# Performance work log

Measured on AMD Instinct MI355X. Metric: run time of the kernel, lower is better.

The kernel has to match this reference:

```python
import jax, jax.numpy as jnp
import numpy as np

NUM_CLASSES = 32
MAX_DET = 100        # max_detections
CONF = 0.25          # conf_threshold
IOU_THR = 0.45       # iou_threshold
BATCH = 64
ANCHORS = 8400


def setup_inputs() -> dict:
    key = jax.random.key(0)
    # raw YOLO head output [B, 4+num_classes, anchors]; uniform [0,1) so boxes
    # (normalized cx,cy,w,h) and class scores are in valid range.
    yolo_output = jax.random.uniform(key, (BATCH, 4 + NUM_CLASSES, ANCHORS), dtype=jnp.float32)
    return {"yolo_output": yolo_output}


def _iou_one_vs_all(box, boxes):
    # box: [4] (ymin,xmin,ymax,xmax); boxes: [A,4]
    y1 = jnp.maximum(box[0], boxes[:, 0])
    x1 = jnp.maximum(box[1], boxes[:, 1])
    y2 = jnp.minimum(box[2], boxes[:, 2])
    x2 = jnp.minimum(box[3], boxes[:, 3])
    inter = jnp.maximum(y2 - y1, 0.0) * jnp.maximum(x2 - x1, 0.0)
    area_a = (box[2] - box[0]) * (box[3] - box[1])
    area_b = (boxes[:, 2] - boxes[:, 0]) * (boxes[:, 3] - boxes[:, 1])
    union = area_a + area_b - inter
    return jnp.where(union > 0.0, inter / union, 0.0)


def _nms_one_image(boxes, classes, scores):
    # Greedy hard NMS, equivalent to tf.image.non_max_suppression followed by
    # gather + zero-pad to MAX_DET. `scores` already has sub-threshold anchors
    # masked to -1 (emulating boolean_mask by threshold).
    def step(sc, _):
        idx = jnp.argmax(sc)
        s = sc[idx]
        b = boxes[idx]
        c = classes[idx]
        ok = s > 0.0  # any remaining valid candidate?
        iou = _iou_one_vs_all(b, boxes)
        new_sc = jnp.where(iou > IOU_THR, -1.0, sc).at[idx].set(-1.0)
        sc = jnp.where(ok, new_sc, sc)
        out = (jnp.where(ok, b, 0.0), jnp.where(ok, c, 0.0), jnp.where(ok, s, 0.0), ok)
        return sc, out

    _, (sel_boxes, sel_classes, sel_scores, valid) = jax.lax.scan(
        step, scores, None, length=MAX_DET)
    num_det = jnp.sum(valid.astype(jnp.float32))
    return sel_boxes, sel_classes, sel_scores, num_det


def _forward(yolo_output):
    # [B, 36, A] -> [B, A, 36]
    t = jnp.transpose(yolo_output, (0, 2, 1))
    boxes_raw = t[..., :4]                      # cx, cy, w, h (normalized)
    class_scores = t[..., 4:]                   # [B, A, num_classes]
    best_scores = jnp.max(class_scores, axis=-1)
    best_classes = jax.lax.stop_gradient(
        jnp.argmax(class_scores, axis=-1).astype(jnp.float32))
    xc, yc, w, h = (boxes_raw[..., 0], boxes_raw[..., 1],
                    boxes_raw[..., 2], boxes_raw[..., 3])
    clip = lambda v: jnp.clip(v, 0.0, 1.0)
    # TF order: [ymin, xmin, ymax, xmax]
    corner = jnp.stack([clip(yc - h * 0.5), clip(xc - w * 0.5),
                        clip(yc + h * 0.5), clip(xc + w * 0.5)], axis=-1)
    # confidence threshold: mask out instead of boolean_mask (jit-friendly)
    masked_scores = jnp.where(best_scores >= CONF, best_scores, -1.0)
    det_boxes, det_classes, det_scores, num_det = jax.vmap(_nms_one_image)(
        corner, best_classes, masked_scores)
    return det_boxes, det_classes, det_scores, num_det


def reference(yolo_output):
    # Returns (detection_boxes [B,100,4], detection_classes [B,100],
    #          detection_scores [B,100], num_detections [B])
    return _forward(yolo_output)
```

## Files before the change

kernel.cpp:

```cpp
#include <hip/hip_runtime.h>

#define BATCH   64
#define CHANS   36
#define ANCH    8400
#define NCLS    32
#define MAXDET  100
#define CONF    0.25f
#define KTOP    512
#define NBUCK   2048
#define BUCK0   (0x3E800000u >> 13)

typedef unsigned long long u64;
typedef unsigned int       u32;

__device__ __forceinline__ bool iou_gt(float ay1, float ax1, float ay2, float ax2, float aar,
                                       float by1, float bx1, float by2, float bx2, float bar,
                                       double M) {
#pragma clang fp contract(off)
    float iy1 = fmaxf(ay1, by1), ix1 = fmaxf(ax1, bx1);
    float iy2 = fminf(ay2, by2), ix2 = fminf(ax2, bx2);
    float inter = fmaxf(iy2 - iy1, 0.f) * fmaxf(ix2 - ix1, 0.f);
    float uni = (aar + bar) - inter;
    return (double)inter > M * (double)uni;
}

__global__ __launch_bounds__(256) void yolo_prep(const float* __restrict__ in,
                                                 float4* __restrict__ wbox,
                                                 u64* __restrict__ wk64,
                                                 u32* __restrict__ hist) {
#pragma clang fp contract(off)
    const int G = ANCH / 4;
    int g = blockIdx.x * 256 + threadIdx.x;
    int b = blockIdx.y;
    bool act = (g < G);

    __shared__ u32 lh[NBUCK];
    for (int i = threadIdx.x; i < NBUCK; i += 256) lh[i] = 0u;
    __syncthreads();

    if (act) {
        const float4* p = (const float4*)(in + (size_t)b * (CHANS * ANCH));
        float4 xc = p[0 * G + g], yc = p[1 * G + g], ww = p[2 * G + g], hh = p[3 * G + g];
        float4 best = p[4 * G + g];
        uint4 bc = make_uint4(0, 0, 0, 0);
#pragma unroll
        for (int k = 1; k < NCLS; ++k) {
            float4 v = p[(4 + k) * G + g];
            if (v.x > best.x) { best.x = v.x; bc.x = k; }
            if (v.y > best.y) { best.y = v.y; bc.y = k; }
            if (v.z > best.z) { best.z = v.z; bc.z = k; }
            if (v.w > best.w) { best.w = v.w; bc.w = k; }
        }
        int a0 = b * ANCH + 4 * g;
        u64* wk = wk64 + (size_t)b * ANCH + 4 * g;
#define PREP_C(C, I)                                                          \
        {                                                                     \
            float Y1 = fminf(fmaxf(yc.C - hh.C * 0.5f, 0.f), 1.f);            \
            float X1 = fminf(fmaxf(xc.C - ww.C * 0.5f, 0.f), 1.f);            \
            float Y2 = fminf(fmaxf(yc.C + hh.C * 0.5f, 0.f), 1.f);            \
            float X2 = fminf(fmaxf(xc.C + ww.C * 0.5f, 0.f), 1.f);            \
            wbox[a0 + I] = make_float4(Y1, X1, Y2, X2);                       \
            u64 kv = 0ull;                                                    \
            if (best.C >= CONF) {                                             \
                u32 sb = __float_as_uint(best.C);                             \
                kv = ((u64)sb << 32) |                                        \
                     ((u64)(16383 - (4 * g + I)) << 18) | (u64)(bc.C & 31u);  \
                atomicAdd(&lh[(sb >> 13) - BUCK0], 1u);                       \
            }                                                                 \
            wk[I] = kv;                                                       \
        }
        PREP_C(x, 0) PREP_C(y, 1) PREP_C(z, 2) PREP_C(w, 3)
#undef PREP_C
    }
    __syncthreads();
    u32* gh = hist + (size_t)b * NBUCK;
    for (int i = threadIdx.x; i < NBUCK; i += 256) {
        u32 c = lh[i];
        if (c) atomicAdd(&gh[i], c);
    }
}

__global__ __launch_bounds__(256) void yolo_taupart(u64* __restrict__ wk64,
                                                    const u32* __restrict__ hist,
                                                    u64* __restrict__ gkA,
                                                    u32* __restrict__ meta) {
    int b = blockIdx.x, t = threadIdx.x;
    const u32* gh = hist + (size_t)b * NBUCK;

    __shared__ u32 wsum[4];
    __shared__ u32 bestP;
    __shared__ u32 shT;
    __shared__ u32 curA;
    __shared__ u32 staub;
    if (t == 0) { bestP = 0u; curA = 0u; }
    __syncthreads();

    u32 c[8], sloc[8];
    u32 run = 0;
#pragma unroll
    for (int q = 0; q < 8; ++q) {
        int r = t * 8 + q;
        c[q] = gh[2047 - r];
        run += c[q];
        sloc[q] = run;
    }
    u32 Su = run;
    u32 x = Su;
#pragma unroll
    for (int d = 1; d < 64; d <<= 1) {
        u32 y = __shfl_up(x, d, 64);
        if ((t & 63) >= d) x += y;
    }
    if ((t & 63) == 63) wsum[t >> 6] = x;
    __syncthreads();
    u32 base = 0;
    for (int w = 0; w < (t >> 6); ++w) base += wsum[w];
    u32 excl = base + x - Su;

    u32 mypk = 0;
#pragma unroll
    for (int q = 0; q < 8; ++q) {
        u32 inc = excl + sloc[q];
        if (inc <= (u32)KTOP) {
            u32 pk = (inc << 11) | (u32)(t * 8 + q);
            if (pk > mypk) mypk = pk;
        }
    }
    if (mypk) atomicMax(&bestP, mypk);
    if (t == 255) shT = excl + Su;
    __syncthreads();
    if (t == 0) {
        u32 bp = bestP, K, taub;
        if (bp == 0u) { K = 0u; taub = (u32)NBUCK; }
        else { K = bp >> 11; taub = 2047u - (bp & 0x7FFu); }
        meta[b * 4 + 0] = K;
        meta[b * 4 + 1] = shT;
        meta[b * 4 + 2] = taub;
        staub = taub;
    }
    __syncthreads();
    u32 taub = staub;

    const u64* gk = wk64 + (size_t)b * ANCH;
    u64* ga = gkA + (size_t)b * KTOP;
    for (int j = 0; j < 33; ++j) {
        int a = t + j * 256;
        if (a < ANCH) {
            u64 k = gk[a];
            if (k != 0ull && ((u32)(k >> 45) - BUCK0) >= taub) {
                u32 slot = atomicAdd(&curA, 1u);
                ga[slot] = k;
            }
        }
    }
}

__global__ __launch_bounds__(256) void yolo_matrix(const float4* __restrict__ wbox,
                                                   const u64* __restrict__ gkA,
                                                   const u32* __restrict__ meta,
                                                   u64* __restrict__ gS) {
#pragma clang fp contract(off)
    const double M = (double)0.45f + 0x1p-26;
    int b = blockIdx.x, t = threadIdx.x;
    const float4* bx = wbox + (size_t)b * ANCH;
    const u64* ga = gkA + (size_t)b * KTOP;
    int K = (int)meta[b * 4 + 0];

    __shared__ u64    ck[KTOP];
    __shared__ float4 cb[KTOP];
    __shared__ float  ca[KTOP];

    for (int i = t; i < KTOP; i += 256) {
        u64 k = (i < K) ? ga[i] : 0ull;
        ck[i] = k;
        float4 bb = make_float4(0.f, 0.f, 0.f, 0.f);
        if (k != 0ull) {
            int a = 16383 - (int)((k >> 18) & 0x3FFFull);
            bb = bx[a];
        }
        cb[i] = bb;
        ca[i] = (bb.z - bb.x) * (bb.w - bb.y);
    }
    __syncthreads();

    int row = blockIdx.y * 64 + (t >> 2);
    int seg = t & 3;
    u64 kr = ck[row];
    float4 rb = cb[row];
    float rar = ca[row];
    u64 w0 = 0ull, w1 = 0ull;
    int base0 = seg * 128;
#pragma unroll 4
    for (int j = 0; j < 64; ++j) {
        {
            int i = base0 + j;
            u64 ki = ck[i];
            if ((ki > kr) && iou_gt(cb[i].x, cb[i].y, cb[i].z, cb[i].w, ca[i],
                                    rb.x, rb.y, rb.z, rb.w, rar, M))
                w0 |= 1ull << j;
        }
        {
            int i = base0 + 64 + j;
            u64 ki = ck[i];
            if ((ki > kr) && iou_gt(cb[i].x, cb[i].y, cb[i].z, cb[i].w, ca[i],
                                    rb.x, rb.y, rb.z, rb.w, rar, M))
                w1 |= 1ull << j;
        }
    }
    ulonglong2 wv; wv.x = w0; wv.y = w1;
    *(ulonglong2*)&gS[(size_t)b * (KTOP * 8) + (size_t)row * 8 + seg * 2] = wv;
}

__global__ __launch_bounds__(256) void yolo_resolve(const float4* __restrict__ wbox,
                                                    u64* __restrict__ wk64,
                                                    const u64* __restrict__ gkA,
                                                    const u64* __restrict__ gS,
                                                    const u32* __restrict__ meta,
                                                    float* __restrict__ out) {
#pragma clang fp contract(off)
    const double M = (double)0.45f + 0x1p-26;
    int b = blockIdx.x, t = threadIdx.x;
    const float4* bx = wbox + (size_t)b * ANCH;
    u64* gk = wk64 + (size_t)b * ANCH;
    const u64* ga = gkA + (size_t)b * KTOP;
    int K = (int)meta[b * 4 + 0], T = (int)meta[b * 4 + 1];
    u32 taub = meta[b * 4 + 2];

    __shared__ u64   ck[KTOP];
    __shared__ u64   SP[KTOP * 9];
    __shared__ u64   selKey[KTOP];
    __shared__ float selb[MAXDET][5];
    __shared__ u64   redm[4];
    __shared__ int   selTotS;

    float* outBox = out + (size_t)b * (MAXDET * 4);
    float* outCls = out + (size_t)(BATCH * MAXDET * 4) + b * MAXDET;
    float* outScr = out + (size_t)(BATCH * MAXDET * 5) + b * MAXDET;
    float* outNum = out + (size_t)(BATCH * MAXDET * 6) + b;

    for (int i = t; i < KTOP; i += 256) ck[i] = (i < K) ? ga[i] : 0ull;
    const u64* gSb = gS + (size_t)b * (KTOP * 8);
    for (int i = t; i < KTOP * 8; i += 256) SP[(i >> 3) * 9 + (i & 7)] = gSb[i];
    __syncthreads();

    u64 S[8];
#pragma unroll
    for (int w = 0; w < 8; ++w) S[w] = 0ull;
    if (t < 64) {
        int L = t;
        u64 U[8];
#pragma unroll
        for (int w = 0; w < 8; ++w) U[w] = __ballot(ck[(w << 6) + L] != 0ull);
        for (int it = 0; it < KTOP; ++it) {
            if (!(U[0] | U[1] | U[2] | U[3] | U[4] | U[5] | U[6] | U[7])) break;
            u64 D[8];
#pragma unroll
            for (int w = 0; w < 8; ++w) {
                const u64* rm = &SP[((w << 6) + L) * 9];
                u64 pend = (rm[0] & U[0]) | (rm[1] & U[1]) | (rm[2] & U[2]) | (rm[3] & U[3])
                         | (rm[4] & U[4]) | (rm[5] & U[5]) | (rm[6] & U[6]) | (rm[7] & U[7]);
                D[w] = __ballot(((U[w] >> L) & 1ull) && (pend == 0ull));
            }
#pragma unroll
            for (int w = 0; w < 8; ++w) { S[w] |= D[w]; U[w] &= ~D[w]; }
#pragma unroll
            for (int w = 0; w < 8; ++w) {
                const u64* rm = &SP[((w << 6) + L) * 9];
                u64 hit = (rm[0] & D[0]) | (rm[1] & D[1]) | (rm[2] & D[2]) | (rm[3] & D[3])
                        | (rm[4] & D[4]) | (rm[5] & D[5]) | (rm[6] & D[6]) | (rm[7] & D[7]);
                U[w] &= ~__ballot(((U[w] >> L) & 1ull) && (hit != 0ull));
            }
        }
        if (t == 0) {
            int c = 0;
#pragma unroll
            for (int w = 0; w < 8; ++w) c += (int)__popcll(S[w]);
            selTotS = c;
        }
    }
    __syncthreads();

    if (t < 64) {
        int L = t, base = 0;
#pragma unroll
        for (int w = 0; w < 8; ++w) {
            u64 Sw = S[w];
            if ((Sw >> L) & 1ull) {
                int r = base + (int)__popcll(Sw & ((1ull << L) - 1ull));
                selKey[r] = ck[(w << 6) + L];
            }
            base += (int)__popcll(Sw);
        }
    }
    __syncthreads();

    int sTot = selTotS;
    int s = sTot < MAXDET ? sTot : MAXDET;

    if (t < 64) {
        int L = t;
#pragma unroll
        for (int w = 0; w < 8; ++w) {
            if ((S[w] >> L) & 1ull) {
                u64 myk = ck[(w << 6) + L];
                int pos = 0;
                for (int j = 0; j < sTot; ++j) pos += (selKey[j] > myk) ? 1 : 0;
                if (pos < MAXDET) {
                    int a = 16383 - (int)((myk >> 18) & 0x3FFFull);
                    float4 bb = bx[a];
                    outScr[pos] = __uint_as_float((u32)(myk >> 32));
                    outCls[pos] = (float)((u32)myk & 31u);
                    outBox[pos * 4 + 0] = bb.x; outBox[pos * 4 + 1] = bb.y;
                    outBox[pos * 4 + 2] = bb.z; outBox[pos * 4 + 3] = bb.w;
                    selb[pos][0] = bb.x; selb[pos][1] = bb.y; selb[pos][2] = bb.z;
                    selb[pos][3] = bb.w; selb[pos][4] = (bb.z - bb.x) * (bb.w - bb.y);
                }
            }
        }
    }
    __syncthreads();

    if (s < MAXDET && T > K) {
        for (int i = t; i < ANCH; i += 256) {
            u64 k = gk[i];
            if (k != 0ull) {
                if (((u32)(k >> 45) - BUCK0) >= taub) { gk[i] = 0ull; continue; }
                int a = 16383 - (int)((k >> 18) & 0x3FFFull);
                float4 bb = bx[a];
                float ar = (bb.z - bb.x) * (bb.w - bb.y);
                for (int j = 0; j < s; ++j) {
                    if (iou_gt(selb[j][0], selb[j][1], selb[j][2], selb[j][3], selb[j][4],
                               bb.x, bb.y, bb.z, bb.w, ar, M)) { gk[i] = 0ull; break; }
                }
            }
        }
        __syncthreads();
        while (s < MAXDET) {
            u64 best = 0ull;
            for (int i = t; i < ANCH; i += 256) { u64 k = gk[i]; if (k > best) best = k; }
#pragma unroll
            for (int sh = 1; sh < 64; sh <<= 1) {
                u64 o = __shfl_xor(best, sh, 64);
                if (o > best) best = o;
            }
            if ((t & 63) == 0) redm[t >> 6] = best;
            __syncthreads();
            best = redm[0];
            for (int w = 1; w < 4; ++w) if (redm[w] > best) best = redm[w];
            if (best == 0ull) break;
            int a = 16383 - (int)((best >> 18) & 0x3FFFull);
            float4 nb = bx[a];
            float nar = (nb.z - nb.x) * (nb.w - nb.y);
            if (t == 0) {
                outScr[s] = __uint_as_float((u32)(best >> 32));
                outCls[s] = (float)((u32)best & 31u);
                outBox[s * 4 + 0] = nb.x; outBox[s * 4 + 1] = nb.y;
                outBox[s * 4 + 2] = nb.z; outBox[s * 4 + 3] = nb.w;
            }
            for (int i = t; i < ANCH; i += 256) {
                u64 k = gk[i];
                if (k != 0ull) {
                    if (k == best) gk[i] = 0ull;
                    else {
                        int a2 = 16383 - (int)((k >> 18) & 0x3FFFull);
                        float4 bb = bx[a2];
                        float ar = (bb.z - bb.x) * (bb.w - bb.y);
                        if (iou_gt(nb.x, nb.y, nb.z, nb.w, nar,
                                   bb.x, bb.y, bb.z, bb.w, ar, M)) gk[i] = 0ull;
                    }
                }
            }
            ++s;
            __syncthreads();
        }
    }

    for (int q = s + t; q < MAXDET; q += 256) {
        outScr[q] = 0.f; outCls[q] = 0.f;
        outBox[q * 4 + 0] = 0.f; outBox[q * 4 + 1] = 0.f;
        outBox[q * 4 + 2] = 0.f; outBox[q * 4 + 3] = 0.f;
    }
    if (t == 0) *outNum = (float)s;
}

extern "C" void kernel_launch(void* const* d_in, const int* in_sizes, int n_in,
                              void* d_out, int out_size, void* d_ws, size_t ws_size,
                              hipStream_t stream) {
    const float* in = (const float*)d_in[0];
    float* out = (float*)d_out;
    char* w = (char*)d_ws;
    float4* wbox = (float4*)w;
    u64*    wk64 = (u64*)(w + 8601600);
    u64*    gkA  = (u64*)(w + 8601600 + 4300800);
    u64*    gS   = (u64*)(w + 8601600 + 4300800 + 262144);
    u32*    hist = (u32*)(w + 8601600 + 4300800 + 262144 + 2097152);
    u32*    meta = (u32*)(w + 8601600 + 4300800 + 262144 + 2097152 + 524288);

    hipMemsetAsync(hist, 0, (size_t)BATCH * NBUCK * 4, stream);
    dim3 gp((ANCH / 4 + 255) / 256, BATCH);
    yolo_prep<<<gp, 256, 0, stream>>>(in, wbox, wk64, hist);
    yolo_taupart<<<BATCH, 256, 0, stream>>>(wk64, hist, gkA, meta);
    yolo_matrix<<<dim3(BATCH, 8), 256, 0, stream>>>(wbox, gkA, meta, gS);
    yolo_resolve<<<BATCH, 256, 0, stream>>>(wbox, wk64, gkA, gS, meta, out);
}
```

Before: 184.3 us.

## Fuse tau-partition, IoU matrix and resolve into one per-image NMS kernel

Merges the taupart, matrix and resolve kernels into a single per-image kernel that keeps the candidate keys and the suppression bitmask in shared memory rather than round-tripping through global buffers. Per-block histograms are written directly and summed in the consumer, which removes the memset and the global atomics. Boxes are no longer stored as a precomputed array and are recomputed from the raw input on demand. The trade-off is that the IoU matrix now runs on only 64 blocks instead of 512, and the larger shared-memory footprint lowers occupancy.

Result: slower. 299.2 us (+62.3%).

```diff
diff --git a/kernel.cpp b/kernel.cpp
--- a/kernel.cpp
+++ b/kernel.cpp
@@ -9,6 +9,7 @@
 #define KTOP    512
 #define NBUCK   2048
 #define BUCK0   (0x3E800000u >> 13)
+#define PBLK    9
 
 typedef unsigned long long u64;
 typedef unsigned int       u32;
@@ -24,23 +25,32 @@
     return (double)inter > M * (double)uni;
 }
 
+__device__ __forceinline__ float4 load_box(const float* __restrict__ inb, int a) {
+#pragma clang fp contract(off)
+    float xc = inb[0 * ANCH + a], yc = inb[1 * ANCH + a];
+    float w  = inb[2 * ANCH + a], h  = inb[3 * ANCH + a];
+    float4 r;
+    r.x = fminf(fmaxf(yc - h * 0.5f, 0.f), 1.f);
+    r.y = fminf(fmaxf(xc - w * 0.5f, 0.f), 1.f);
+    r.z = fminf(fmaxf(yc + h * 0.5f, 0.f), 1.f);
+    r.w = fminf(fmaxf(xc + w * 0.5f, 0.f), 1.f);
+    return r;
+}
+
 __global__ __launch_bounds__(256) void yolo_prep(const float* __restrict__ in,
-                                                 float4* __restrict__ wbox,
                                                  u64* __restrict__ wk64,
-                                                 u32* __restrict__ hist) {
+                                                 u32* __restrict__ histp) {
 #pragma clang fp contract(off)
     const int G = ANCH / 4;
     int g = blockIdx.x * 256 + threadIdx.x;
     int b = blockIdx.y;
-    bool act = (g < G);
 
     __shared__ u32 lh[NBUCK];
     for (int i = threadIdx.x; i < NBUCK; i += 256) lh[i] = 0u;
     __syncthreads();
 
-    if (act) {
+    if (g < G) {
         const float4* p = (const float4*)(in + (size_t)b * (CHANS * ANCH));
-        float4 xc = p[0 * G + g], yc = p[1 * G + g], ww = p[2 * G + g], hh = p[3 * G + g];
         float4 best = p[4 * G + g];
         uint4 bc = make_uint4(0, 0, 0, 0);
 #pragma unroll
@@ -51,15 +61,9 @@
             if (v.z > best.z) { best.z = v.z; bc.z = k; }
             if (v.w > best.w) { best.w = v.w; bc.w = k; }
         }
-        int a0 = b * ANCH + 4 * g;
         u64* wk = wk64 + (size_t)b * ANCH + 4 * g;
 #define PREP_C(C, I)                                                          \
         {                                                                     \
-            float Y1 = fminf(fmaxf(yc.C - hh.C * 0.5f, 0.f), 1.f);            \
-            float X1 = fminf(fmaxf(xc.C - ww.C * 0.5f, 0.f), 1.f);            \
-            float Y2 = fminf(fmaxf(yc.C + hh.C * 0.5f, 0.f), 1.f);            \
-            float X2 = fminf(fmaxf(xc.C + ww.C * 0.5f, 0.f), 1.f);            \
-            wbox[a0 + I] = make_float4(Y1, X1, Y2, X2);                       \
             u64 kv = 0ull;                                                    \
             if (best.C >= CONF) {                                             \
                 u32 sb = __float_as_uint(best.C);                             \
@@ -73,35 +77,55 @@
 #undef PREP_C
     }
     __syncthreads();
-    u32* gh = hist + (size_t)b * NBUCK;
-    for (int i = threadIdx.x; i < NBUCK; i += 256) {
-        u32 c = lh[i];
-        if (c) atomicAdd(&gh[i], c);
-    }
-}
-
-__global__ __launch_bounds__(256) void yolo_taupart(u64* __restrict__ wk64,
-                                                    const u32* __restrict__ hist,
-                                                    u64* __restrict__ gkA,
-                                                    u32* __restrict__ meta) {
+    u32* gh = histp + ((size_t)b * PBLK + blockIdx.x) * NBUCK;
+    for (int i = threadIdx.x; i < NBUCK; i += 256) gh[i] = lh[i];
+}
+
+__global__ __launch_bounds__(256) void yolo_nms(const float* __restrict__ in,
+                                                u64* __restrict__ wk64,
+                                                const u32* __restrict__ histp,
+                                                float* __restrict__ out) {
+#pragma clang fp contract(off)
+    const double M = (double)0.45f + 0x1p-26;
     int b = blockIdx.x, t = threadIdx.x;
-    const u32* gh = hist + (size_t)b * NBUCK;
-
-    __shared__ u32 wsum[4];
-    __shared__ u32 bestP;
-    __shared__ u32 shT;
-    __shared__ u32 curA;
-    __shared__ u32 staub;
+    const float* inb = in + (size_t)b * (CHANS * ANCH);
+    u64* gk = wk64 + (size_t)b * ANCH;
+
+    __shared__ u32    hist[NBUCK];
+    __shared__ u64    ck[KTOP];
+    __shared__ float4 cb[KTOP];
+    __shared__ float  ca[KTOP];
+    __shared__ u64    SP[KTOP * 9];
+    __shared__ u64    selKey[KTOP];
+    __shared__ float  selb[MAXDET][5];
+    __shared__ u64    redm[4];
+    __shared__ u32    wsum[4];
+    __shared__ u32    bestP, shT, curA, staub, shK;
+    __shared__ int    selTotS;
+
+    float* outBox = out + (size_t)b * (MAXDET * 4);
+    float* outCls = out + (size_t)(BATCH * MAXDET * 4) + b * MAXDET;
+    float* outScr = out + (size_t)(BATCH * MAXDET * 5) + b * MAXDET;
+    float* outNum = out + (size_t)(BATCH * MAXDET * 6) + b;
+
     if (t == 0) { bestP = 0u; curA = 0u; }
-    __syncthreads();
-
-    u32 c[8], sloc[8];
+
+    const u32* ghp = histp + (size_t)b * PBLK * NBUCK;
+    for (int i = t; i < NBUCK; i += 256) {
+        u32 c = 0;
+#pragma unroll
+        for (int j = 0; j < PBLK; ++j) c += ghp[j * NBUCK + i];
+        hist[i] = c;
+    }
+    __syncthreads();
+
+    u32 c8[8], sloc[8];
     u32 run = 0;
 #pragma unroll
     for (int q = 0; q < 8; ++q) {
         int r = t * 8 + q;
-        c[q] = gh[2047 - r];
-        run += c[q];
+        c8[q] = hist[2047 - r];
+        run += c8[q];
         sloc[q] = run;
     }
     u32 Su = run;
@@ -130,117 +154,61 @@
     if (t == 255) shT = excl + Su;
     __syncthreads();
     if (t == 0) {
-        u32 bp = bestP, K, taub;
-        if (bp == 0u) { K = 0u; taub = (u32)NBUCK; }
-        else { K = bp >> 11; taub = 2047u - (bp & 0x7FFu); }
-        meta[b * 4 + 0] = K;
-        meta[b * 4 + 1] = shT;
-        meta[b * 4 + 2] = taub;
-        staub = taub;
+        u32 bp = bestP;
+        if (bp == 0u) { shK = 0u; staub = (u32)NBUCK; }
+        else { shK = bp >> 11; staub = 2047u - (bp & 0x7FFu); }
     }
     __syncthreads();
     u32 taub = staub;
-
-    const u64* gk = wk64 + (size_t)b * ANCH;
-    u64* ga = gkA + (size_t)b * KTOP;
+    int K = (int)shK, T = (int)shT;
+
     for (int j = 0; j < 33; ++j) {
         int a = t + j * 256;
         if (a < ANCH) {
             u64 k = gk[a];
             if (k != 0ull && ((u32)(k >> 45) - BUCK0) >= taub) {
                 u32 slot = atomicAdd(&curA, 1u);
-                ga[slot] = k;
-            }
-        }
-    }
-}
-
-__global__ __launch_bounds__(256) void yolo_matrix(const float4* __restrict__ wbox,
-                                                   const u64* __restrict__ gkA,
-                                                   const u32* __restrict__ meta,
-                                                   u64* __restrict__ gS) {
-#pragma clang fp contract(off)
-    const double M = (double)0.45f + 0x1p-26;
-    int b = blockIdx.x, t = threadIdx.x;
-    const float4* bx = wbox + (size_t)b * ANCH;
-    const u64* ga = gkA + (size_t)b * KTOP;
-    int K = (int)meta[b * 4 + 0];
-
-    __shared__ u64    ck[KTOP];
-    __shared__ float4 cb[KTOP];
-    __shared__ float  ca[KTOP];
+                if (slot < (u32)KTOP) ck[slot] = k;
+            }
+        }
+    }
+    __syncthreads();
+    for (int i = K + t; i < KTOP; i += 256) ck[i] = 0ull;
+    __syncthreads();
 
     for (int i = t; i < KTOP; i += 256) {
-        u64 k = (i < K) ? ga[i] : 0ull;
-        ck[i] = k;
+        u64 k = ck[i];
         float4 bb = make_float4(0.f, 0.f, 0.f, 0.f);
         if (k != 0ull) {
             int a = 16383 - (int)((k >> 18) & 0x3FFFull);
-            bb = bx[a];
+            bb = load_box(inb, a);
         }
         cb[i] = bb;
         ca[i] = (bb.z - bb.x) * (bb.w - bb.y);
     }
     __syncthreads();
 
-    int row = blockIdx.y * 64 + (t >> 2);
-    int seg = t & 3;
-    u64 kr = ck[row];
-    float4 rb = cb[row];
-    float rar = ca[row];
-    u64 w0 = 0ull, w1 = 0ull;
-    int base0 = seg * 128;
+#pragma unroll
+    for (int rr = 0; rr < 2; ++rr) {
+        int row = t + rr * 256;
+        u64 kr = ck[row];
+        float4 rb = cb[row];
+        float rar = ca[row];
+#pragma unroll
+        for (int w = 0; w < 8; ++w) {
+            u64 word = 0ull;
+            int base0 = w << 6;
 #pragma unroll 4
-    for (int j = 0; j < 64; ++j) {
-        {
-            int i = base0 + j;
-            u64 ki = ck[i];
-            if ((ki > kr) && iou_gt(cb[i].x, cb[i].y, cb[i].z, cb[i].w, ca[i],
-                                    rb.x, rb.y, rb.z, rb.w, rar, M))
-                w0 |= 1ull << j;
-        }
-        {
-            int i = base0 + 64 + j;
-            u64 ki = ck[i];
-            if ((ki > kr) && iou_gt(cb[i].x, cb[i].y, cb[i].z, cb[i].w, ca[i],
-                                    rb.x, rb.y, rb.z, rb.w, rar, M))
-                w1 |= 1ull << j;
-        }
-    }
-    ulonglong2 wv; wv.x = w0; wv.y = w1;
-    *(ulonglong2*)&gS[(size_t)b * (KTOP * 8) + (size_t)row * 8 + seg * 2] = wv;
-}
-
-__global__ __launch_bounds__(256) void yolo_resolve(const float4* __restrict__ wbox,
-                                                    u64* __restrict__ wk64,
-                                                    const u64* __restrict__ gkA,
-                                                    const u64* __restrict__ gS,
-                                                    const u32* __restrict__ meta,
-                                                    float* __restrict__ out) {
-#pragma clang fp contract(off)
-    const double M = (double)0.45f + 0x1p-26;
-    int b = blockIdx.x, t = threadIdx.x;
-    const float4* bx = wbox + (size_t)b * ANCH;
-    u64* gk = wk64 + (size_t)b * ANCH;
-    const u64* ga = gkA + (size_t)b * KTOP;
-    int K = (int)meta[b * 4 + 0], T = (int)meta[b * 4 + 1];
-    u32 taub = meta[b * 4 + 2];
-
-    __shared__ u64   ck[KTOP];
-    __shared__ u64   SP[KTOP * 9];
-    __shared__ u64   selKey[KTOP];
-    __shared__ float selb[MAXDET][5];
-    __shared__ u64   redm[4];
-    __shared__ int   selTotS;
-
-    float* outBox = out + (size_t)b * (MAXDET * 4);
-    float* outCls = out + (size_t)(BATCH * MAXDET * 4) + b * MAXDET;
-    float* outScr = out + (size_t)(BATCH * MAXDET * 5) + b * MAXDET;
-    float* outNum = out + (size_t)(BATCH * MAXDET * 6) + b;
-
-    for (int i = t; i < KTOP; i += 256) ck[i] = (i < K) ? ga[i] : 0ull;
-    const u64* gSb = gS + (size_t)b * (KTOP * 8);
-    for (int i = t; i < KTOP * 8; i += 256) SP[(i >> 3) * 9 + (i & 7)] = gSb[i];
+            for (int j2 = 0; j2 < 64; ++j2) {
+                int i = base0 + j2;
+                u64 ki = ck[i];
+                if ((ki > kr) && iou_gt(cb[i].x, cb[i].y, cb[i].z, cb[i].w, ca[i],
+                                        rb.x, rb.y, rb.z, rb.w, rar, M))
+                    word |= 1ull << j2;
+            }
+            SP[row * 9 + w] = word;
+        }
+    }
     __syncthreads();
 
     u64 S[8];
@@ -281,15 +249,15 @@
     __syncthreads();
 
     if (t < 64) {
-        int L = t, base = 0;
+        int L = t, kbase = 0;
 #pragma unroll
         for (int w = 0; w < 8; ++w) {
             u64 Sw = S[w];
             if ((Sw >> L) & 1ull) {
-                int r = base + (int)__popcll(Sw & ((1ull << L) - 1ull));
+                int r = kbase + (int)__popcll(Sw & ((1ull << L) - 1ull));
                 selKey[r] = ck[(w << 6) + L];
             }
-            base += (int)__popcll(Sw);
+            kbase += (int)__popcll(Sw);
         }
     }
     __syncthreads();
@@ -307,7 +275,7 @@
                 for (int j = 0; j < sTot; ++j) pos += (selKey[j] > myk) ? 1 : 0;
                 if (pos < MAXDET) {
                     int a = 16383 - (int)((myk >> 18) & 0x3FFFull);
-                    float4 bb = bx[a];
+                    float4 bb = load_box(inb, a);
                     outScr[pos] = __uint_as_float((u32)(myk >> 32));
                     outCls[pos] = (float)((u32)myk & 31u);
                     outBox[pos * 4 + 0] = bb.x; outBox[pos * 4 + 1] = bb.y;
@@ -326,7 +294,7 @@
             if (k != 0ull) {
                 if (((u32)(k >> 45) - BUCK0) >= taub) { gk[i] = 0ull; continue; }
                 int a = 16383 - (int)((k >> 18) & 0x3FFFull);
-                float4 bb = bx[a];
+                float4 bb = load_box(inb, a);
                 float ar = (bb.z - bb.x) * (bb.w - bb.y);
                 for (int j = 0; j < s; ++j) {
                     if (iou_gt(selb[j][0], selb[j][1], selb[j][2], selb[j][3], selb[j][4],
@@ -349,7 +317,7 @@
             for (int w = 1; w < 4; ++w) if (redm[w] > best) best = redm[w];
             if (best == 0ull) break;
             int a = 16383 - (int)((best >> 18) & 0x3FFFull);
-            float4 nb = bx[a];
+            float4 nb = load_box(inb, a);
             float nar = (nb.z - nb.x) * (nb.w - nb.y);
             if (t == 0) {
                 outScr[s] = __uint_as_float((u32)(best >> 32));
@@ -363,7 +331,7 @@
                     if (k == best) gk[i] = 0ull;
                     else {
                         int a2 = 16383 - (int)((k >> 18) & 0x3FFFull);
-                        float4 bb = bx[a2];
+                        float4 bb = load_box(inb, a2);
                         float ar = (bb.z - bb.x) * (bb.w - bb.y);
                         if (iou_gt(nb.x, nb.y, nb.z, nb.w, nar,
                                    bb.x, bb.y, bb.z, bb.w, ar, M)) gk[i] = 0ull;
@@ -389,17 +357,9 @@
     const float* in = (const float*)d_in[0];
     float* out = (float*)d_out;
     char* w = (char*)d_ws;
-    float4* wbox = (float4*)w;
-    u64*    wk64 = (u64*)(w + 8601600);
-    u64*    gkA  = (u64*)(w + 8601600 + 4300800);
-    u64*    gS   = (u64*)(w + 8601600 + 4300800 + 262144);
-    u32*    hist = (u32*)(w + 8601600 + 4300800 + 262144 + 2097152);
-    u32*    meta = (u32*)(w + 8601600 + 4300800 + 262144 + 2097152 + 524288);
-
-    hipMemsetAsync(hist, 0, (size_t)BATCH * NBUCK * 4, stream);
-    dim3 gp((ANCH / 4 + 255) / 256, BATCH);
-    yolo_prep<<<gp, 256, 0, stream>>>(in, wbox, wk64, hist);
-    yolo_taupart<<<BATCH, 256, 0, stream>>>(wk64, hist, gkA, meta);
-    yolo_matrix<<<dim3(BATCH, 8), 256, 0, stream>>>(wbox, gkA, meta, gS);
-    yolo_resolve<<<BATCH, 256, 0, stream>>>(wbox, wk64, gkA, gS, meta, out);
-}
+    u64* wk64  = (u64*)w;
+    u32* histp = (u32*)(w + 4300800);
+
+    yolo_prep<<<dim3(PBLK, BATCH), 256, 0, stream>>>(in, wk64, histp);
+    yolo_nms<<<BATCH, 256, 0, stream>>>(in, wk64, histp, out);
+}
```
